# Kernel optimization log

Hardware: AMD Instinct MI355X
Metric: run time of the kernel (lower is better)

## Reference

```python
import jax, jax.numpy as jnp
import numpy as np
from jax import lax

B, C, O, K, L, W = 32, 128, 128, 3, 4096, 1
PAD, DIL = 1, 1


def _conv(x, w, b):
    # x: [B,C,H,W], w: [O,C,K,1] -> [B,O,H,W] (zeros padding, stride 1)
    y = lax.conv_general_dilated(x, w, window_strides=(1, 1),
                                 padding=[(PAD, PAD), (0, 0)],
                                 rhs_dilation=(DIL, 1),
                                 dimension_numbers=('NCHW', 'OIHW', 'NCHW'))
    return y + b[None, :, None, None]


def setup_inputs() -> dict:
    key = jax.random.key(0)
    ks = jax.random.split(key, 6)
    x = jax.random.normal(ks[0], (B, C, L, W), dtype=jnp.float32)
    # offset/modulator convs are zero-init in torch; use small random values to
    # exercise the deformable gather path (represents a trained state)
    w_off = jax.random.normal(ks[1], (2 * K, C, K, 1), dtype=jnp.float32) * 0.01
    b_off = jax.random.normal(ks[2], (2 * K,), dtype=jnp.float32) * 0.1
    w_mod = jax.random.normal(ks[3], (K, C, K, 1), dtype=jnp.float32) * 0.01
    b_mod = jax.random.normal(ks[4], (K,), dtype=jnp.float32) * 0.1
    w_reg = jax.random.normal(ks[5], (O, C, K, 1), dtype=jnp.float32) * (1.0 / np.sqrt(C * K))
    return {"x": x, "w_off": w_off, "b_off": b_off,
            "w_mod": w_mod, "b_mod": b_mod, "w_reg": w_reg}


def reference(x, w_off, b_off, w_mod, b_mod, w_reg):
    b, c, h, w = x.shape
    max_offset = max(h, w) / 4.0
    offset = jnp.clip(_conv(x, w_off, b_off), -max_offset, max_offset)  # [B,2K,H,W]
    mask = 2.0 * jax.nn.sigmoid(_conv(x, w_mod, b_mod))                 # [B,K,H,W]

    off = offset.reshape(b, K, 2, h, w)
    off_y, off_x = off[:, :, 0], off[:, :, 1]                           # [B,K,H,W]

    # sampling positions (stride=1, pad_w=0, kw=1)
    base_y = (-PAD + jnp.arange(K, dtype=jnp.float32)[:, None] * DIL
              + jnp.arange(h, dtype=jnp.float32)[None, :])              # [K,H]
    py = base_y[None, :, :, None] + off_y                               # [B,K,H,W]
    px = jnp.arange(w, dtype=jnp.float32)[None, None, None, :] + off_x  # [B,K,H,W]

    y0 = jnp.floor(py); x0 = jnp.floor(px)
    iy0 = y0.astype(jnp.int32); ix0 = x0.astype(jnp.int32)
    wy1 = py - y0; wy0 = 1.0 - wy1
    wx1 = px - x0; wx0 = 1.0 - wx1

    def gather(iy, ix):
        iyc = jnp.clip(iy, 0, h - 1)
        ixc = jnp.clip(ix, 0, w - 1)
        # per-batch gather: xb [C,H,W], idx [K,H,W] -> [C,K,H,W]
        return jax.vmap(lambda xb, yb, xb_i: xb[:, yb, xb_i])(x, iyc, ixc)

    acc = jnp.zeros((b, c, K, h, w), dtype=x.dtype)
    corners = [(iy0, ix0, wy0 * wx0), (iy0, ix0 + 1, wy0 * wx1),
               (iy0 + 1, ix0, wy1 * wx0), (iy0 + 1, ix0 + 1, wy1 * wx1)]
    for iy, ix, wgt in corners:
        valid = ((iy >= 0) & (iy < h) & (ix >= 0) & (ix < w)).astype(x.dtype)
        acc = acc + gather(iy, ix) * (wgt * valid)[:, None]  # [B,C,K,H,W]

    val = acc * mask[:, None]                                 # modulated samples
    out = jnp.einsum('bckhw,ock->bohw', val, w_reg[:, :, :, 0])
    return out
```

## Files before the change

kernel.cpp:

```cpp
#include <hip/hip_runtime.h>
#include <hip/hip_bf16.h>
#include <math.h>


typedef __attribute__((ext_vector_type(8))) short bf16x8;
typedef __attribute__((ext_vector_type(4))) float f32x4;
typedef float f32x2u __attribute__((ext_vector_type(2), aligned(4)));

#define WIN 160
#define WP32 162

static __device__ inline unsigned short f2bf(float f) {
    __hip_bfloat16 h = __float2bfloat16(f);
    union { __hip_bfloat16 b; unsigned short u; } cv;
    cv.b = h;
    return cv.u;
}
static __device__ inline unsigned pk2(float a, float b) {
    return (unsigned)f2bf(a) | ((unsigned)f2bf(b) << 16);
}

__global__ __launch_bounds__(256) void k_wra(const float* __restrict__ w_reg,
                                             const float* __restrict__ w_off,
                                             const float* __restrict__ w_mod,
                                             unsigned short* __restrict__ WrA,
                                             float* __restrict__ wT) {
    int t = blockIdx.x * 256 + threadIdx.x;
    if (t < 8 * 12 * 64 * 8) {
        int e  = t & 7;
        int l  = (t >> 3) & 63;
        int ms = t >> 9;
        int m  = ms / 12;
        int s  = ms - m * 12;
        int o  = m * 16 + (l & 15);
        int kc = s * 32 + ((l >> 4) & 3) * 8 + e;
        int tap = kc >> 7;
        int c   = kc & 127;
        WrA[t] = f2bf(w_reg[(o * 128 + c) * 3 + tap]);
    } else if (t < 8 * 12 * 64 * 8 + 128 * 27) {
        int u = t - 8 * 12 * 64 * 8;
        int c = u / 27, r = u - c * 27;
        int ch = r / 3, tap = r - ch * 3;
        wT[c * 32 + r] = (ch < 6) ? w_off[(ch * 128 + c) * 3 + tap]
                                  : w_mod[((ch - 6) * 128 + c) * 3 + tap];
    }
}

__global__ __launch_bounds__(512) void k_prep(const float* __restrict__ x,
                                              const float* __restrict__ wT,
                                              const float* __restrict__ b_off,
                                              const float* __restrict__ b_mod,
                                              int* __restrict__ addr2,
                                              float* __restrict__ wae,
                                              float* __restrict__ wbe) {
    __shared__ float red[7 * 64 * 19];
    int t = threadIdx.x;
    int lane = t & 63;
    int wv = t >> 6;
    int b = blockIdx.y;
    int i = blockIdx.x * 128 + lane * 2;

    int c0 = __builtin_amdgcn_readfirstlane(wv) * 16;

    float acc[18];
#pragma unroll
    for (int z = 0; z < 18; ++z) acc[z] = 0.f;

    const float* xr = x + (size_t)b * 524288 + (size_t)c0 * 4096;
    const float* wbase = wT + c0 * 32;
#pragma unroll 2
    for (int c = 0; c < 16; ++c) {
        const float* row = xr + (size_t)c * 4096;
        f32x2u v = *(const f32x2u*)(row + i);
        float lm = row[max(i - 1, 0)];
        float rp = row[min(i + 2, 4095)];
        float left  = (i > 0)        ? lm : 0.f;
        float right = (i + 2 < 4096) ? rp : 0.f;
        const float* wrow = wbase + c * 32;
#pragma unroll
        for (int ch = 0; ch < 9; ++ch) {
            float w0 = wrow[ch * 3 + 0];
            float w1 = wrow[ch * 3 + 1];
            float w2 = wrow[ch * 3 + 2];
            acc[ch * 2 + 0] += left * w0 + v.x * w1 + v.y  * w2;
            acc[ch * 2 + 1] += v.x  * w0 + v.y * w1 + right * w2;
        }
    }

    if (wv > 0) {
        float* r = &red[((wv - 1) * 64 + lane) * 19];
#pragma unroll
        for (int z = 0; z < 18; ++z) r[z] = acc[z];
    }
    __syncthreads();
    if (wv != 0) return;

#pragma unroll
    for (int p = 0; p < 7; ++p) {
        const float* r = &red[(p * 64 + lane) * 19];
#pragma unroll
        for (int z = 0; z < 18; ++z) acc[z] += r[z];
    }

#pragma unroll
    for (int k = 0; k < 3; ++k) {
        int   av[2];
        float wav[2], wbv[2];
#pragma unroll
        for (int ii = 0; ii < 2; ++ii) {
            float offy = acc[(2 * k) * 2 + ii]     + b_off[2 * k];
            float offx = acc[(2 * k + 1) * 2 + ii] + b_off[2 * k + 1];
            offy = fminf(fmaxf(offy, -1024.f), 1024.f);
            offx = fminf(fmaxf(offx, -1024.f), 1024.f);
            float am = acc[(6 + k) * 2 + ii] + b_mod[k];
            float m  = 2.f / (1.f + expf(-am));

            float py = (float)(i + ii - 1 + k) + offy;
            float y0 = floorf(py);
            int   iy0 = (int)y0;
            float wy1 = py - y0, wy0 = 1.f - wy1;
            float x0f = floorf(offx);
            int   ix0 = (int)x0f;
            float wx1 = offx - x0f, wx0 = 1.f - wx1;

            float sx = (ix0 == 0) ? wx0 : ((ix0 == -1) ? wx1 : 0.f);
            float scal = m * sx;

            float wAv = (iy0 >= 0 && iy0 < 4096)  ? scal * wy0 : 0.f;
            float wBv = (iy0 >= -1 && iy0 < 4095) ? scal * wy1 : 0.f;

            int addr = min(max(iy0, 0), 4094);
            bool eq = (iy0 == addr);
            wav[ii] = eq ? wAv : (iy0 == -1   ? wBv : 0.f);
            wbv[ii] = eq ? wBv : (iy0 == 4095 ? wAv : 0.f);
            av[ii] = addr;
        }
        int j = (b * 3 + k) * 4096 + i;
        *(int2*)(addr2 + j)  = make_int2(av[0], av[1]);
        *(f32x2u*)(wae + j)  = (f32x2u){wav[0], wav[1]};
        *(f32x2u*)(wbe + j)  = (f32x2u){wbv[0], wbv[1]};
    }
}

__global__ __launch_bounds__(512) void k_fused(const unsigned short* __restrict__ WrA,
                                               const float* __restrict__ x,
                                               const int* __restrict__ addr2,
                                               const float* __restrict__ wae,
                                               const float* __restrict__ wbe,
                                               float* __restrict__ out) {
    __shared__ unsigned win32[32 * WP32];
    __shared__ short Bl[8][3][512];
    int t = threadIdx.x;
    int l = t & 63;
    int w = t >> 6;
    int b  = blockIdx.y;
    int ib = blockIdx.x;
    int q = l >> 4;
    int il = l & 15;
    int i0t = ib * 128;
    int i0p = i0t + w * 16 + il;
    int wsod = i0t - 16;
    if (wsod > 4096 - WIN) wsod = 4096 - WIN;
    if (wsod < 0) wsod = 0;
    const float* xb = x + (size_t)b * 524288;
    const bf16x8* Ag = (const bf16x8*)WrA;

    int   a_[3];
    float wa_[3], wb_[3];
    bool  okw[3];
#pragma unroll
    for (int k = 0; k < 3; ++k) {
        int j = (b * 3 + k) * 4096 + i0p;
        int a = addr2[j];
        a_[k]  = a;
        wa_[k] = wae[j];
        wb_[k] = wbe[j];
        okw[k] = (bool)__all(a >= wsod && a <= wsod + WIN - 2);
    }

    f32x4 acc[8];
#pragma unroll
    for (int f = 0; f < 8; ++f) acc[f] = (f32x4){0.f, 0.f, 0.f, 0.f};

#pragma unroll
    for (int it = 0; it < 3; ++it) {
        int idx = it * 512 + t;
        if (idx < 1280) {
            int r = idx / 40, cp = idx - r * 40;
            const float* row = xb + (size_t)r * 4096;
            int c0 = wsod + cp * 4;
            float4 v = *(const float4*)(row + c0);
            float nx = row[min(c0 + 4, 4095)];
            unsigned* d = &win32[r * WP32 + cp * 4];
            *(uint2*)(d)     = make_uint2(pk2(v.x, v.y), pk2(v.y, v.z));
            *(uint2*)(d + 2) = make_uint2(pk2(v.z, v.w), pk2(v.w, nx));
        }
    }
    __syncthreads();

    for (int cc = 0; cc < 4; ++cc) {
        int cb = cc * 32;

        bf16x8 Areg[3];
#pragma unroll
        for (int k = 0; k < 3; ++k)
            Areg[k] = Ag[(w * 12 + k * 4 + cc) * 64 + l];

#pragma unroll
        for (int k = 0; k < 3; ++k) {
            float v[8];
            float wa = wa_[k], wb = wb_[k];
            if (okw[k]) {
                int pos = a_[k] - wsod;
#pragma unroll
                for (int e = 0; e < 8; ++e) {
                    unsigned u = win32[(q * 8 + e) * WP32 + pos];
                    float lo = __uint_as_float(u << 16);
                    float hi = __uint_as_float(u & 0xffff0000u);
                    v[e] = wa * lo + wb * hi;
                }
            } else {
                int a = a_[k];
#pragma unroll
                for (int e = 0; e < 8; ++e) {
                    const float* row = xb + (size_t)(cb + q * 8 + e) * 4096;
                    f32x2u p2 = *(const f32x2u*)(row + a);
                    v[e] = wa * p2.x + wb * p2.y;
                }
            }
            bf16x8 Bv;
#pragma unroll
            for (int e = 0; e < 8; ++e) Bv[e] = (short)f2bf(v[e]);
            *(bf16x8*)&Bl[w][k][l * 8] = Bv;
        }

        uint4 sp[3];
        if (cc < 3) {
#pragma unroll
            for (int it = 0; it < 3; ++it) {
                int idx = it * 512 + t;
                if (idx < 1280) {
                    int r = idx / 40, cp = idx - r * 40;
                    const float* row = xb + (size_t)(cb + 32 + r) * 4096;
                    int c0 = wsod + cp * 4;
                    float4 v = *(const float4*)(row + c0);
                    float nx = row[min(c0 + 4, 4095)];
                    sp[it] = make_uint4(pk2(v.x, v.y), pk2(v.y, v.z),
                                        pk2(v.z, v.w), pk2(v.w, nx));
                }
            }
        }

        asm volatile("s_waitcnt lgkmcnt(0)" ::: "memory");
        __builtin_amdgcn_sched_barrier(0);
        __builtin_amdgcn_s_barrier();

        __builtin_amdgcn_s_setprio(1);
#pragma unroll
        for (int f = 0; f < 8; ++f) {
#pragma unroll
            for (int k = 0; k < 3; ++k) {
                bf16x8 Bv = *(const bf16x8*)&Bl[f][k][l * 8];
                acc[f] = __builtin_amdgcn_mfma_f32_16x16x32_bf16(Areg[k], Bv, acc[f], 0, 0, 0);
            }
        }
        __builtin_amdgcn_s_setprio(0);

        if (cc < 3) {
#pragma unroll
            for (int it = 0; it < 3; ++it) {
                int idx = it * 512 + t;
                if (idx < 1280) {
                    int r = idx / 40, cp = idx - r * 40;
                    unsigned* d = &win32[r * WP32 + cp * 4];
                    *(uint2*)(d)     = make_uint2(sp[it].x, sp[it].y);
                    *(uint2*)(d + 2) = make_uint2(sp[it].z, sp[it].w);
                }
            }
            asm volatile("s_waitcnt lgkmcnt(0)" ::: "memory");
            __builtin_amdgcn_sched_barrier(0);
            __builtin_amdgcn_s_barrier();
        }
    }

    int r0 = q * 4;
#pragma unroll
    for (int f = 0; f < 8; ++f) {
#pragma unroll
        for (int r = 0; r < 4; ++r) {
            int o = w * 16 + r0 + r;
            out[((size_t)(b * 128 + o)) * 4096 + i0t + f * 16 + il] = acc[f][r];
        }
    }
}

extern "C" void kernel_launch(void* const* d_in, const int* in_sizes, int n_in,
                              void* d_out, int out_size, void* d_ws, size_t ws_size,
                              hipStream_t stream) {
    const float* x     = (const float*)d_in[0];
    const float* w_off = (const float*)d_in[1];
    const float* b_off = (const float*)d_in[2];
    const float* w_mod = (const float*)d_in[3];
    const float* b_mod = (const float*)d_in[4];
    const float* w_reg = (const float*)d_in[5];
    float* out = (float*)d_out;

    char* ws = (char*)d_ws;
    unsigned short* WrA = (unsigned short*)(ws);
    float* wT    = (float*)(ws + 98304);
    int*   addr2 = (int*)  (ws + 131072);
    float* wae   = (float*)(ws + 1703936);
    float* wbe   = (float*)(ws + 3276800);

    k_wra<<<206, 256, 0, stream>>>(w_reg, w_off, w_mod, WrA, wT);
    k_prep<<<dim3(32, 32), 512, 0, stream>>>(x, wT, b_off, b_mod,
                                             addr2, wae, wbe);
    k_fused<<<dim3(32, 32), 512, 0, stream>>>(WrA, x, addr2, wae, wbe, out);
}
```

Measured before the change: 67.42 us.

## Switch fused GEMM to 32x32x16 bf16 MFMA with 32x64 wave tiles

The fused deformable-gather GEMM moves from 16x16x32 MFMA (each wave owning 16 output channels across all 128 positions) to 32x32x16 MFMA, where each wave owns a 32-channel by 64-position tile. The weight prepack, the LDS B-tile layout and the gather/channel assignment per wave are reorganized to match, and the A fragments are now loaded inside the MFMA loop instead of being hoisted per chunk. The aim is fewer, larger MFMA instructions and less LDS B-operand traffic per FLOP. In exchange it adds global A loads in the hot loop and a different output store pattern.

```diff
diff --git a/kernel.cpp b/kernel.cpp
--- a/kernel.cpp
+++ b/kernel.cpp
@@ -3,8 +3,9 @@
 #include <math.h>
 
 
-typedef __attribute__((ext_vector_type(8))) short bf16x8;
-typedef __attribute__((ext_vector_type(4))) float f32x4;
+typedef __attribute__((ext_vector_type(8)))  short bf16x8;
+typedef __attribute__((ext_vector_type(4)))  float f32x4;
+typedef __attribute__((ext_vector_type(16))) float f32x16;
 typedef float f32x2u __attribute__((ext_vector_type(2), aligned(4)));
 
 #define WIN 160
@@ -26,19 +27,19 @@
                                              unsigned short* __restrict__ WrA,
                                              float* __restrict__ wT) {
     int t = blockIdx.x * 256 + threadIdx.x;
-    if (t < 8 * 12 * 64 * 8) {
+    if (t < 49152) {
         int e  = t & 7;
         int l  = (t >> 3) & 63;
-        int ms = t >> 9;
-        int m  = ms / 12;
-        int s  = ms - m * 12;
-        int o  = m * 16 + (l & 15);
-        int kc = s * 32 + ((l >> 4) & 3) * 8 + e;
+        int os = t >> 9;
+        int ot = os / 24;
+        int sg = os - ot * 24;
+        int o  = ot * 32 + (l & 31);
+        int kc = sg * 16 + ((l >> 5) & 1) * 8 + e;
         int tap = kc >> 7;
         int c   = kc & 127;
         WrA[t] = f2bf(w_reg[(o * 128 + c) * 3 + tap]);
-    } else if (t < 8 * 12 * 64 * 8 + 128 * 27) {
-        int u = t - 8 * 12 * 64 * 8;
+    } else if (t < 49152 + 128 * 27) {
+        int u = t - 49152;
         int c = u / 27, r = u - c * 27;
         int ch = r / 3, tap = r - ch * 3;
         wT[c * 32 + r] = (ch < 6) ? w_off[(ch * 128 + c) * 3 + tap]
@@ -149,16 +150,20 @@
                                                const float* __restrict__ wbe,
                                                float* __restrict__ out) {
     __shared__ unsigned win32[32 * WP32];
-    __shared__ short Bl[8][3][512];
+    __shared__ short Bl[4][6][512];
     int t = threadIdx.x;
     int l = t & 63;
     int w = t >> 6;
     int b  = blockIdx.y;
     int ib = blockIdx.x;
-    int q = l >> 4;
-    int il = l & 15;
+    int cl = l & 31;
+    int eh = (l >> 5) & 1;
     int i0t = ib * 128;
-    int i0p = i0t + w * 16 + il;
+    int itp = w >> 1;
+    int hp  = w & 1;
+    int ot  = w >> 1;
+    int ih  = w & 1;
+    int i0p = i0t + itp * 32 + cl;
     int wsod = i0t - 16;
     if (wsod > 4096 - WIN) wsod = 4096 - WIN;
     if (wsod < 0) wsod = 0;
@@ -178,9 +183,11 @@
         okw[k] = (bool)__all(a >= wsod && a <= wsod + WIN - 2);
     }
 
-    f32x4 acc[8];
-#pragma unroll
-    for (int f = 0; f < 8; ++f) acc[f] = (f32x4){0.f, 0.f, 0.f, 0.f};
+    f32x16 acc[2];
+#pragma unroll
+    for (int j = 0; j < 2; ++j)
+#pragma unroll
+        for (int r = 0; r < 16; ++r) acc[j][r] = 0.f;
 
 #pragma unroll
     for (int it = 0; it < 3; ++it) {
@@ -201,11 +208,6 @@
     for (int cc = 0; cc < 4; ++cc) {
         int cb = cc * 32;
 
-        bf16x8 Areg[3];
-#pragma unroll
-        for (int k = 0; k < 3; ++k)
-            Areg[k] = Ag[(w * 12 + k * 4 + cc) * 64 + l];
-
 #pragma unroll
         for (int k = 0; k < 3; ++k) {
             float v[8];
@@ -214,7 +216,8 @@
                 int pos = a_[k] - wsod;
 #pragma unroll
                 for (int e = 0; e < 8; ++e) {
-                    unsigned u = win32[(q * 8 + e) * WP32 + pos];
+                    int row = hp * 16 + eh * 8 + e;
+                    unsigned u = win32[row * WP32 + pos];
                     float lo = __uint_as_float(u << 16);
                     float hi = __uint_as_float(u & 0xffff0000u);
                     v[e] = wa * lo + wb * hi;
@@ -223,7 +226,8 @@
                 int a = a_[k];
 #pragma unroll
                 for (int e = 0; e < 8; ++e) {
-                    const float* row = xb + (size_t)(cb + q * 8 + e) * 4096;
+                    int c = cb + hp * 16 + eh * 8 + e;
+                    const float* row = xb + (size_t)c * 4096;
                     f32x2u p2 = *(const f32x2u*)(row + a);
                     v[e] = wa * p2.x + wb * p2.y;
                 }
@@ -231,7 +235,7 @@
             bf16x8 Bv;
 #pragma unroll
             for (int e = 0; e < 8; ++e) Bv[e] = (short)f2bf(v[e]);
-            *(bf16x8*)&Bl[w][k][l * 8] = Bv;
+            *(bf16x8*)&Bl[itp][k * 2 + hp][l * 8] = Bv;
         }
 
         uint4 sp[3];
@@ -257,11 +261,15 @@
 
         __builtin_amdgcn_s_setprio(1);
 #pragma unroll
-        for (int f = 0; f < 8; ++f) {
-#pragma unroll
-            for (int k = 0; k < 3; ++k) {
-                bf16x8 Bv = *(const bf16x8*)&Bl[f][k][l * 8];
-                acc[f] = __builtin_amdgcn_mfma_f32_16x16x32_bf16(Areg[k], Bv, acc[f], 0, 0, 0);
+        for (int tap = 0; tap < 3; ++tap) {
+#pragma unroll
+            for (int h = 0; h < 2; ++h) {
+                bf16x8 A = Ag[(ot * 24 + tap * 8 + cc * 2 + h) * 64 + l];
+#pragma unroll
+                for (int j = 0; j < 2; ++j) {
+                    bf16x8 Bv = *(const bf16x8*)&Bl[2 * ih + j][tap * 2 + h][l * 8];
+                    acc[j] = __builtin_amdgcn_mfma_f32_32x32x16_bf16(A, Bv, acc[j], 0, 0, 0);
+                }
             }
         }
         __builtin_amdgcn_s_setprio(0);
@@ -283,13 +291,15 @@
         }
     }
 
-    int r0 = q * 4;
-#pragma unroll
-    for (int f = 0; f < 8; ++f) {
-#pragma unroll
-        for (int r = 0; r < 4; ++r) {
-            int o = w * 16 + r0 + r;
-            out[((size_t)(b * 128 + o)) * 4096 + i0t + f * 16 + il] = acc[f][r];
+    int rbase = 4 * eh;
+#pragma unroll
+    for (int j = 0; j < 2; ++j) {
+        size_t ibase = (size_t)i0t + (2 * ih + j) * 32 + cl;
+#pragma unroll
+        for (int r = 0; r < 16; ++r) {
+            int rowc = (r & 3) + 8 * (r >> 2) + rbase;
+            int o = ot * 32 + rowc;
+            out[((size_t)(b * 128 + o)) * 4096 + ibase] = acc[j][r];
         }
     }
 }
```

After: 73.12 us. 8.5% more time.
